# Kernel tuning notes

Measured on AMD Instinct MI355X. Metric: run time of the kernel, lower is better.

The kernel has to match this reference:

```python
import jax, jax.numpy as jnp
import numpy as np

B, S, DMAX, NMEL, DM, K = 8, 100, 12, 80, 128, 9
T = S * DMAX  # 1200 max mel frames
EPS = 1e-5  # BatchNorm eps (eval mode, running_mean=0, running_var=1)


def setup_inputs() -> dict:
    key = jax.random.key(0)
    ks = jax.random.split(key, 16)
    durations = jax.random.randint(ks[0], (B, S), 4, DMAX + 1).astype(jnp.int32)
    mel_len = jnp.sum(durations, axis=1).astype(jnp.int32)
    src_len = jnp.full((B,), S, dtype=jnp.int32)
    mel = jax.random.normal(ks[1], (B, T, NMEL), dtype=jnp.float32)
    # conv stack params (xavier-ish uniform)
    s1 = float(np.sqrt(6.0 / (1 * K + DM * K)))
    w1 = jax.random.uniform(ks[2], (DM, 1, 1, K), minval=-s1, maxval=s1, dtype=jnp.float32)
    g1 = 1.0 + 0.1 * jax.random.normal(ks[3], (DM,), dtype=jnp.float32)
    be1 = 0.1 * jax.random.normal(ks[4], (DM,), dtype=jnp.float32)
    s2 = float(np.sqrt(6.0 / (DM * K + 1 * K)))
    w2 = jax.random.uniform(ks[5], (1, DM, 1, K), minval=-s2, maxval=s2, dtype=jnp.float32)
    g2 = 1.0 + 0.1 * jax.random.normal(ks[6], (1,), dtype=jnp.float32)
    be2 = 0.1 * jax.random.normal(ks[7], (1,), dtype=jnp.float32)
    # BiGRU params (pytorch layout: gates [r|z|n] stacked -> 3*H rows)
    sh = float(1.0 / np.sqrt(DM))
    u = lambda k, shape: jax.random.uniform(k, shape, minval=-sh, maxval=sh, dtype=jnp.float32)
    w_ih_f = u(ks[8], (3 * DM, NMEL)); w_hh_f = u(ks[9], (3 * DM, DM))
    b_ih_f = u(ks[10], (3 * DM,));    b_hh_f = u(ks[11], (3 * DM,))
    w_ih_b = u(ks[12], (3 * DM, NMEL)); w_hh_b = u(ks[13], (3 * DM, DM))
    b_ih_b = u(ks[14], (3 * DM,));    b_hh_b = u(ks[15], (3 * DM,))
    return {"mel": mel, "durations": durations, "mel_len": mel_len, "src_len": src_len,
            "w1": w1, "g1": g1, "be1": be1, "w2": w2, "g2": g2, "be2": be2,
            "w_ih_f": w_ih_f, "w_hh_f": w_hh_f, "b_ih_f": b_ih_f, "b_hh_f": b_hh_f,
            "w_ih_b": w_ih_b, "w_hh_b": w_hh_b, "b_ih_b": b_ih_b, "b_hh_b": b_hh_b}


def _bn_eval(x, g, b):
    # eval-mode BatchNorm2d with running_mean=0, running_var=1; x [B,C,T,M]
    scale = g / jnp.sqrt(1.0 + EPS)
    return x * scale[None, :, None, None] + b[None, :, None, None]


def _gru_scan(xs_seq, reset_seq, w_hh, b_hh):
    # xs_seq [T,B,3H] precomputed input projections; reset_seq [T,B] 1.0 -> reset h to 0
    H = w_hh.shape[1]
    Bn = xs_seq.shape[1]

    def step(h, inp):
        xg, rst = inp
        h = h * (1.0 - rst)[:, None]
        hg = h @ w_hh.T + b_hh
        xr, xz, xn = jnp.split(xg, 3, axis=-1)
        hr, hz, hn = jnp.split(hg, 3, axis=-1)
        r = jax.nn.sigmoid(xr + hr)
        z = jax.nn.sigmoid(xz + hz)
        n = jnp.tanh(xn + r * hn)
        h_new = (1.0 - z) * n + z * h
        return h_new, h_new

    h0 = jnp.zeros((Bn, H), xs_seq.dtype)
    _, hs = jax.lax.scan(step, h0, (xs_seq, reset_seq))
    return hs  # [T,B,H]


def reference(mel, durations, mel_len, src_len, w1, g1, be1, w2, g2, be2,
              w_ih_f, w_hh_f, b_ih_f, b_hh_f, w_ih_b, w_hh_b, b_ih_b, b_hh_b):
    pad = (K - 1) // 2
    # conv stack: kernel (1,K) mixes only the mel-channel axis -> apply to full mel once
    x = mel[:, None, :, :]  # [B,1,T,M]
    x = jax.lax.conv_general_dilated(x, w1, (1, 1), [(0, 0), (pad, pad)])
    x = jax.nn.relu(_bn_eval(x, g1, be1))
    x = jax.lax.conv_general_dilated(x, w2, (1, 1), [(0, 0), (pad, pad)])
    x = jax.nn.relu(_bn_eval(x, g2, be2))
    x = x[:, 0]  # [B,T,M]

    # segment boundaries from durations (all phones valid here, durations > 0)
    cum = jnp.cumsum(durations, axis=1)      # [B,S]
    starts = cum - durations                 # segment start frame per phone
    ends = cum - 1                           # segment end frame per phone
    bidx = jnp.arange(B)[:, None]
    start_mask = jnp.zeros((B, T), x.dtype).at[bidx, starts].set(1.0)
    end_mask = jnp.zeros((B, T), x.dtype).at[bidx, ends].set(1.0)

    # forward direction: reset h at segment starts, read h at segment ends
    xf = jnp.einsum('btm,gm->tbg', x, w_ih_f) + b_ih_f
    Hf = _gru_scan(xf, start_mask.T, w_hh_f, b_hh_f)           # [T,B,H]
    # backward direction: scan reversed time, reset at original segment ends
    xb = jnp.einsum('btm,gm->tbg', x, w_ih_b) + b_ih_b
    Hb = _gru_scan(xb[::-1], end_mask.T[::-1], w_hh_b, b_hh_b)[::-1]  # [T,B,H], orig time

    hf = jnp.take_along_axis(jnp.transpose(Hf, (1, 0, 2)), ends[..., None], axis=1)    # [B,S,H]
    hb = jnp.take_along_axis(jnp.transpose(Hb, (1, 0, 2)), starts[..., None], axis=1)  # [B,S,H]
    out = jnp.concatenate([hf, hb], axis=-1)  # [B,S,2H]
    valid = (jnp.arange(S)[None, :] < src_len[:, None])[..., None]
    return jnp.where(valid, out, 0.0)
```

## Files before the change

kernel.cpp:

```cpp
#include <hip/hip_runtime.h>
#include <math.h>

#define BB   8
#define SS   100
#define TT   1200
#define NM   80
#define DMC  128
#define KK   9
#define G3   384
#define NROW (BB*TT)

typedef __attribute__((ext_vector_type(8))) short short8;
typedef __attribute__((ext_vector_type(4))) float f32x4;
typedef __attribute__((ext_vector_type(2))) float f32x2;

__device__ __forceinline__ float sigmoid_(float v) { return 1.f / (1.f + __expf(-v)); }
__device__ __forceinline__ float tanh_(float v) {
    float a = fabsf(v);
    float e = __expf(-2.f * a);
    float t = (1.f - e) / (1.f + e);
    return copysignf(t, v);
}
__device__ __forceinline__ unsigned short f2bf(float f) {
    unsigned int u = __float_as_uint(f);
    unsigned int r = (u + 0x7fffu + ((u >> 16) & 1u)) >> 16;
    return (unsigned short)r;
}
__device__ __forceinline__ f32x2 pk_fma(f32x2 a, f32x2 b, f32x2 c) {
    f32x2 d;
    asm("v_pk_fma_f32 %0, %1, %2, %3" : "=v"(d) : "v"(a), "v"(b), "v"(c));
    return d;
}
__device__ __forceinline__ f32x2 pk_add(f32x2 a, f32x2 b) {
    f32x2 d;
    asm("v_pk_add_f32 %0, %1, %2" : "=v"(d) : "v"(a), "v"(b));
    return d;
}

__global__ __launch_bounds__(256) void k_convprep(
    const float* __restrict__ mel, const int* __restrict__ mel_len,
    const float* __restrict__ w1, const float* __restrict__ g1, const float* __restrict__ be1,
    const float* __restrict__ w2, const float* __restrict__ g2, const float* __restrict__ be2,
    float* __restrict__ xout,
    const float* __restrict__ whf, const float* __restrict__ whb,
    const float* __restrict__ wif, const float* __restrict__ wib,
    const float* __restrict__ bf, const float* __restrict__ bbv,
    const int* __restrict__ dur,
    unsigned short* __restrict__ wph, unsigned short* __restrict__ wpl,
    unsigned short* __restrict__ wih_h, unsigned short* __restrict__ wih_l,
    float* __restrict__ biasc, int* __restrict__ starts) {
    int bx = blockIdx.x;
    int b  = blockIdx.y;
    int tid = threadIdx.x;

    if (bx >= 600) {
        int pid = (bx - 600) * 8 + b;
        if (pid < 87) {
            int u = pid * 256 + tid;
            if (u < 12288) {
                int idx = u;
                int lane = idx & 63;
                int k32  = (idx >> 6) & 3;
                int tau  = (idx >> 8) % 24;
                int dir  = idx / (24 * 4 * 64);
                const float* w = dir ? whb : whf;
                int gg = tau * 16 + (lane & 15);
                int kbase = k32 * 32 + (lane >> 4) * 8;
#pragma unroll
                for (int j = 0; j < 8; j++) {
                    float v = w[gg * DMC + kbase + j];
                    unsigned short hi = f2bf(v);
                    float hif = __uint_as_float(((unsigned)hi) << 16);
                    unsigned short lo = f2bf(v - hif);
                    wph[idx * 8 + j] = hi;
                    wpl[idx * 8 + j] = lo;
                }
            } else if (u < 21504) {
                int idx = u - 12288;
                int lane = idx & 63;
                int ks   = (idx >> 6) % 3;
                int tau  = idx / (3 * 64);
                int gate = tau * 16 + (lane & 15);
                int kb   = ks * 32 + (lane >> 4) * 8;
                const float* w = (gate < G3) ? (wif + gate * NM) : (wib + (gate - G3) * NM);
#pragma unroll
                for (int j = 0; j < 8; j++) {
                    int k = kb + j;
                    float v = (k < NM) ? w[k] : 0.f;
                    unsigned short hi = f2bf(v);
                    float hif = __uint_as_float(((unsigned)hi) << 16);
                    unsigned short lo = f2bf(v - hif);
                    wih_h[idx * 8 + j] = hi;
                    wih_l[idx * 8 + j] = lo;
                }
            } else {
                int v = u - 21504;
                biasc[v] = (v < G3) ? bf[v] : bbv[v - G3];
            }
        } else {
            int batch = tid >> 5, l = tid & 31;
            int run = 0;
#pragma unroll
            for (int c = 0; c < 4; c++) {
                int s = c * 32 + l;
                int v = (s < SS) ? dur[batch * SS + s] : 0;
                int xv = v;
#pragma unroll
                for (int off = 1; off < 32; off <<= 1) {
                    int t = __shfl_up(xv, off, 32);
                    if (l >= off) xv += t;
                }
                if (s < SS) starts[batch * SS + s] = run + xv - v;
                run += __shfl(xv, 31, 32);
            }
        }
        return;
    }

    int t0 = bx * 2;
    int ml = mel_len[b];
    if (t0 >= ml) return;

    __shared__ __align__(16) f32x2 mp2[96];
    __shared__ __align__(16) f32x2 part2[8][82];

    int mq = tid >> 6, g = tid & 63;
    int ms = 20 * mq;
    const float inv_sqrt = 0.9999950000374997f;

    if (tid < 192) {
        int rr = tid / 96, i = tid - rr * 96;
        float v = 0.f;
        if (i >= 8 && i < 88) v = mel[(b * TT + t0 + rr) * NM + i - 8];
        ((float*)mp2)[i * 2 + rr] = v;
    }
    __syncthreads();

    f32x2 c[20];
#pragma unroll
    for (int m = 0; m < 20; m++) c[m] = (f32x2){0.f, 0.f};

#pragma unroll 1
    for (int dd = 0; dd < 2; dd++) {
        int d = g + 64 * dd;
        float sc = g1[d] * inv_sqrt;
        f32x2 w1p[KK], w2p[KK];
#pragma unroll
        for (int k = 0; k < KK; k++) {
            float a  = w1[d * KK + k] * sc;
            float bq = w2[d * KK + k];
            w1p[k] = (f32x2){a, a};
            w2p[k] = (f32x2){bq, bq};
        }
        float sb = be1[d];
        f32x2 sbp = (f32x2){sb, sb};

        f32x2 mw[12];
        {
            const float4* p4 = (const float4*)(mp2 + ms);
#pragma unroll
            for (int q = 0; q < 6; q++) {
                float4 v = p4[q];
                mw[2 * q]     = (f32x2){v.x, v.y};
                mw[2 * q + 1] = (f32x2){v.z, v.w};
            }
        }
#pragma unroll
        for (int ch = 0; ch < 7; ch++) {
            bool live = true;
            if (ch == 0) live = (mq != 0);
            if (ch == 6) live = (mq != 3);
            if (live) {
                f32x2 yv4[4];
#pragma unroll
                for (int jj = 0; jj < 4; jj++) {
                    f32x2 yv = sbp;
#pragma unroll
                    for (int k = 0; k < KK; k++) yv = pk_fma(w1p[k], mw[jj + k], yv);
                    yv[0] = fmaxf(yv[0], 0.f);
                    yv[1] = fmaxf(yv[1], 0.f);
                    yv4[jj] = yv;
                }
#pragma unroll
                for (int jj = 0; jj < 4; jj++) {
                    int off = ch * 4 + jj;
#pragma unroll
                    for (int k = 0; k < KK; k++) {
                        int mo = off - k;
                        if (mo >= 0 && mo < 20) c[mo] = pk_fma(w2p[k], yv4[jj], c[mo]);
                    }
                }
            }
            if (ch < 6) {
#pragma unroll
                for (int q = 0; q < 8; q++) mw[q] = mw[q + 4];
                const float4* p4 = (const float4*)(mp2 + ms + ch * 4 + 12);
                float4 a0 = p4[0], a1 = p4[1];
                mw[8]  = (f32x2){a0.x, a0.y};
                mw[9]  = (f32x2){a0.z, a0.w};
                mw[10] = (f32x2){a1.x, a1.y};
                mw[11] = (f32x2){a1.z, a1.w};
            }
        }
    }

#pragma unroll
    for (int m = 0; m < 20; m++) {
        f32x2 o;
        o[0] = __shfl_xor(c[m][0], 1);
        o[1] = __shfl_xor(c[m][1], 1);
        c[m] = pk_add(c[m], o);
        o[0] = __shfl_xor(c[m][0], 2);
        o[1] = __shfl_xor(c[m][1], 2);
        c[m] = pk_add(c[m], o);
        o[0] = __shfl_xor(c[m][0], 4);
        o[1] = __shfl_xor(c[m][1], 4);
        c[m] = pk_add(c[m], o);
    }
    if ((g & 7) == 0) {
        int p = g >> 3;
#pragma unroll
        for (int m = 0; m < 20; m++) part2[p][ms + m] = c[m];
    }
    __syncthreads();

    if (tid < 160) {
        int rr = (tid >= 80) ? 1 : 0;
        int m  = tid - 80 * rr;
        int t  = t0 + rr;
        if (t < ml) {
            float s = 0.f;
#pragma unroll
            for (int p = 0; p < 8; p++) s += part2[p][m][rr];
            float v = fmaxf(0.f, fmaf(s, g2[0] * inv_sqrt, be2[0]));
            xout[(b * TT + t) * NM + m] = v;
        }
    }
}

__global__ __launch_bounds__(512, 2) void k_gru(
    const float* __restrict__ x,
    const unsigned short* __restrict__ wph, const unsigned short* __restrict__ wpl,
    const unsigned short* __restrict__ wih_h, const unsigned short* __restrict__ wih_l,
    const float* __restrict__ biasc,
    const int* __restrict__ dur_all, const int* __restrict__ starts,
    const int* __restrict__ src_len,
    const float* __restrict__ bhf, const float* __restrict__ bhb,
    float* __restrict__ out) {
    int sblk = blockIdx.x;
    int b    = blockIdx.y;
    int dir  = blockIdx.z;
    int s0 = sblk * 16;

    __shared__ __align__(16) short8 xbh[12][192];
    __shared__ __align__(16) short8 xbl[12][192];
    __shared__ __align__(16) unsigned short hbh[2][2048];
    __shared__ __align__(16) unsigned short hbl[2][2048];
    __shared__ int sdur[16], sstart[16];

    int tid  = threadIdx.x;
    int wave = tid >> 6, lane = tid & 63;
    int quad = lane >> 4, seg = lane & 15;

    if (tid < 16) {
        int ss = s0 + tid;
        sdur[tid]   = (ss < SS) ? dur_all[b * SS + ss] : 0;
        sstart[tid] = (ss < SS) ? starts[b * SS + ss]  : 0;
    }
    for (int i = tid; i < 2048; i += 512) { hbh[0][i] = 0; hbl[0][i] = 0; }

    short8 Ah[3][4], Al[3][4];
    const short8* wph8 = (const short8*)wph;
    const short8* wpl8 = (const short8*)wpl;
#pragma unroll
    for (int tt = 0; tt < 3; tt++)
#pragma unroll
        for (int k32 = 0; k32 < 4; k32++) {
            int idx = ((dir * 24 + wave + 8 * tt) * 4 + k32) * 64 + lane;
            Ah[tt][k32] = wph8[idx];
            Al[tt][k32] = wpl8[idx];
        }
    short8 Gh[3][3], Gl[3][3];
    const short8* wih_h8 = (const short8*)wih_h;
    const short8* wih_l8 = (const short8*)wih_l;
#pragma unroll
    for (int tt = 0; tt < 3; tt++)
#pragma unroll
        for (int ks = 0; ks < 3; ks++) {
            int idx = ((dir * 24 + wave + 8 * tt) * 3 + ks) * 64 + lane;
            Gh[tt][ks] = wih_h8[idx];
            Gl[tt][ks] = wih_l8[idx];
        }

    int s = s0 + seg;
    int sd = (s < SS) ? dur_all[b * SS + s] : 0;
    int slb = src_len[b];
    const float* bih = biasc + dir * G3;
    const float* bhh = dir ? bhb : bhf;
    int j0 = wave * 16 + quad * 4;
    float4 i_r = *(const float4*)&bih[j0];
    float4 i_z = *(const float4*)&bih[DMC + j0];
    float4 bxn = *(const float4*)&bih[2 * DMC + j0];
    float4 h_r = *(const float4*)&bhh[j0];
    float4 h_z = *(const float4*)&bhh[DMC + j0];
    float4 bhn = *(const float4*)&bhh[2 * DMC + j0];
    float4 br = make_float4(i_r.x + h_r.x, i_r.y + h_r.y, i_r.z + h_r.z, i_r.w + h_r.w);
    float4 bz = make_float4(i_z.x + h_z.x, i_z.y + h_z.y, i_z.z + h_z.z, i_z.w + h_z.w);
    float4 h = make_float4(0.f, 0.f, 0.f, 0.f);

    int idx8 = (j0 >> 5) * 64 + ((j0 >> 3) & 3) * 16 + seg;
    int wbase = idx8 * 8 + (j0 & 7);

    __syncthreads();

#pragma unroll
    for (int q = 0; q < 5; q++) {
        int u = tid + q * 512;
        if (u < 12 * 192) {
            int it  = u / 192;
            int rem = u - it * 192;
            int ks = rem >> 6, ln = rem & 63;
            int sg = ln & 15, qq = ln >> 4;
            int kb = ks * 32 + qq * 8;
            short8 hi8 = {0,0,0,0,0,0,0,0}, lo8 = {0,0,0,0,0,0,0,0};
            int d2 = sdur[sg];
            if (kb < NM && it < d2) {
                int t = dir ? (sstart[sg] + d2 - 1 - it) : (sstart[sg] + it);
                const float* xr = x + (size_t)(b * TT + t) * NM + kb;
#pragma unroll
                for (int j = 0; j < 8; j++) {
                    float v = xr[j];
                    unsigned short hi = f2bf(v);
                    hi8[j] = (short)hi;
                    lo8[j] = (short)f2bf(v - __uint_as_float(((unsigned)hi) << 16));
                }
            }
            xbh[it][rem] = hi8;
            xbl[it][rem] = lo8;
        }
    }
    __syncthreads();

    for (int i = 0; i < 12; i++) {
        int p = i & 1;
        bool act = (i < sd);

        f32x4 axr = (f32x4){0.f,0.f,0.f,0.f};
        f32x4 axz = (f32x4){0.f,0.f,0.f,0.f};
        f32x4 axn = (f32x4){0.f,0.f,0.f,0.f};
        f32x4 ahr = (f32x4){0.f,0.f,0.f,0.f};
        f32x4 ahz = (f32x4){0.f,0.f,0.f,0.f};
        f32x4 ahn = (f32x4){0.f,0.f,0.f,0.f};
#pragma unroll
        for (int ks = 0; ks < 3; ks++) {
            short8 Bxh = xbh[i][ks * 64 + lane];
            short8 Bxl = xbl[i][ks * 64 + lane];
            axr = __builtin_amdgcn_mfma_f32_16x16x32_bf16(Gh[0][ks], Bxh, axr, 0, 0, 0);
            axr = __builtin_amdgcn_mfma_f32_16x16x32_bf16(Gh[0][ks], Bxl, axr, 0, 0, 0);
            axr = __builtin_amdgcn_mfma_f32_16x16x32_bf16(Gl[0][ks], Bxh, axr, 0, 0, 0);
            axz = __builtin_amdgcn_mfma_f32_16x16x32_bf16(Gh[1][ks], Bxh, axz, 0, 0, 0);
            axz = __builtin_amdgcn_mfma_f32_16x16x32_bf16(Gh[1][ks], Bxl, axz, 0, 0, 0);
            axz = __builtin_amdgcn_mfma_f32_16x16x32_bf16(Gl[1][ks], Bxh, axz, 0, 0, 0);
            axn = __builtin_amdgcn_mfma_f32_16x16x32_bf16(Gh[2][ks], Bxh, axn, 0, 0, 0);
            axn = __builtin_amdgcn_mfma_f32_16x16x32_bf16(Gh[2][ks], Bxl, axn, 0, 0, 0);
            axn = __builtin_amdgcn_mfma_f32_16x16x32_bf16(Gl[2][ks], Bxh, axn, 0, 0, 0);
        }
#pragma unroll
        for (int k32 = 0; k32 < 4; k32++) {
            short8 Bh = ((const short8*)hbh[p])[k32 * 64 + lane];
            short8 Bl = ((const short8*)hbl[p])[k32 * 64 + lane];
            ahr = __builtin_amdgcn_mfma_f32_16x16x32_bf16(Ah[0][k32], Bh, ahr, 0, 0, 0);
            ahr = __builtin_amdgcn_mfma_f32_16x16x32_bf16(Ah[0][k32], Bl, ahr, 0, 0, 0);
            ahr = __builtin_amdgcn_mfma_f32_16x16x32_bf16(Al[0][k32], Bh, ahr, 0, 0, 0);
            ahz = __builtin_amdgcn_mfma_f32_16x16x32_bf16(Ah[1][k32], Bh, ahz, 0, 0, 0);
            ahz = __builtin_amdgcn_mfma_f32_16x16x32_bf16(Ah[1][k32], Bl, ahz, 0, 0, 0);
            ahz = __builtin_amdgcn_mfma_f32_16x16x32_bf16(Al[1][k32], Bh, ahz, 0, 0, 0);
            ahn = __builtin_amdgcn_mfma_f32_16x16x32_bf16(Ah[2][k32], Bh, ahn, 0, 0, 0);
            ahn = __builtin_amdgcn_mfma_f32_16x16x32_bf16(Ah[2][k32], Bl, ahn, 0, 0, 0);
            ahn = __builtin_amdgcn_mfma_f32_16x16x32_bf16(Al[2][k32], Bh, ahn, 0, 0, 0);
        }

        if (act) {
            float hv[4]  = {h.x, h.y, h.z, h.w};
            float brv[4] = {br.x, br.y, br.z, br.w};
            float bzv[4] = {bz.x, bz.y, bz.z, bz.w};
            float bxv[4] = {bxn.x, bxn.y, bxn.z, bxn.w};
            float bhv[4] = {bhn.x, bhn.y, bhn.z, bhn.w};
#pragma unroll
            for (int cmp = 0; cmp < 4; cmp++) {
                float r = sigmoid_(axr[cmp] + ahr[cmp] + brv[cmp]);
                float z = sigmoid_(axz[cmp] + ahz[cmp] + bzv[cmp]);
                float n = tanh_(axn[cmp] + bxv[cmp] + r * (ahn[cmp] + bhv[cmp]));
                hv[cmp] = (1.f - z) * n + z * hv[cmp];
            }
            h = make_float4(hv[0], hv[1], hv[2], hv[3]);
            if (i == sd - 1) {
                float4 vout = (s < slb) ? h : make_float4(0.f, 0.f, 0.f, 0.f);
                *(float4*)&out[(b * SS + s) * (2 * DMC) + dir * DMC + j0] = vout;
            }
        }

        {
            float hv[4] = {h.x, h.y, h.z, h.w};
            unsigned short hs_[4], ls_[4];
#pragma unroll
            for (int cmp = 0; cmp < 4; cmp++) {
                unsigned short hi = f2bf(hv[cmp]);
                float hif = __uint_as_float(((unsigned)hi) << 16);
                hs_[cmp] = hi;
                ls_[cmp] = f2bf(hv[cmp] - hif);
            }
            *(ushort4*)&hbh[1 - p][wbase] = make_ushort4(hs_[0], hs_[1], hs_[2], hs_[3]);
            *(ushort4*)&hbl[1 - p][wbase] = make_ushort4(ls_[0], ls_[1], ls_[2], ls_[3]);
        }
        __syncthreads();
    }
}

extern "C" void kernel_launch(void* const* d_in, const int* in_sizes, int n_in,
                              void* d_out, int out_size, void* d_ws, size_t ws_size,
                              hipStream_t stream) {
    const float* mel      = (const float*)d_in[0];
    const int*   durations= (const int*)  d_in[1];
    const int*   mel_len  = (const int*)  d_in[2];
    const int*   src_len  = (const int*)  d_in[3];
    const float* w1       = (const float*)d_in[4];
    const float* g1       = (const float*)d_in[5];
    const float* be1      = (const float*)d_in[6];
    const float* w2       = (const float*)d_in[7];
    const float* g2       = (const float*)d_in[8];
    const float* be2      = (const float*)d_in[9];
    const float* w_ih_f   = (const float*)d_in[10];
    const float* w_hh_f   = (const float*)d_in[11];
    const float* b_ih_f   = (const float*)d_in[12];
    const float* b_hh_f   = (const float*)d_in[13];
    const float* w_ih_b   = (const float*)d_in[14];
    const float* w_hh_b   = (const float*)d_in[15];
    const float* b_ih_b   = (const float*)d_in[16];
    const float* b_hh_b   = (const float*)d_in[17];
    float* out = (float*)d_out;

    float* x    = (float*)d_ws;
    unsigned short* wph   = (unsigned short*)(x + NROW * NM);
    unsigned short* wpl   = wph + 2 * 24 * 4 * 64 * 8;
    unsigned short* wih_h = wpl + 2 * 24 * 4 * 64 * 8;
    unsigned short* wih_l = wih_h + 48 * 3 * 64 * 8;
    float* biasc = (float*)(wih_l + 48 * 3 * 64 * 8);
    int*   starts= (int*)(biasc + 768);

    k_convprep<<<dim3(611, BB), 256, 0, stream>>>(
        mel, mel_len, w1, g1, be1, w2, g2, be2, x,
        w_hh_f, w_hh_b, w_ih_f, w_ih_b, b_ih_f, b_ih_b,
        durations, wph, wpl, wih_h, wih_l, biasc, starts);
    k_gru<<<dim3(7, 8, 2), 512, 0, stream>>>(x, wph, wpl, wih_h, wih_l, biasc,
                                             durations, starts, src_len,
                                             b_hh_f, b_hh_b, out);
}
```

Baseline: 154.3 us.

## Fuse conv and GRU stages into one persistent cooperative kernel

Merges the conv-stack/weight-prep kernel and the BiGRU kernel into a single cooperative launch of 256 persistent 512-thread blocks. Each block loops over frame pairs for the conv, with the conv weights held in registers across iterations, then a subset of blocks runs the GRU after a grid-wide sync. The shared memory of the two phases is overlaid in a union. This removes one kernel launch and the gap between the two kernels, and reuses the per-channel conv weights across rows. In exchange it needs a grid barrier, and the GRU phase only occupies 112 of the 256 blocks.

Result: slower. 277.6 us (+80.0%).

```diff
diff --git a/kernel.cpp b/kernel.cpp
--- a/kernel.cpp
+++ b/kernel.cpp
@@ -1,5 +1,8 @@
 #include <hip/hip_runtime.h>
+#include <hip/hip_cooperative_groups.h>
 #include <math.h>
+
+namespace cg = cooperative_groups;
 
 #define BB   8
 #define SS   100
@@ -37,7 +40,20 @@
     return d;
 }
 
-__global__ __launch_bounds__(256) void k_convprep(
+struct ConvSh {
+    f32x2 mp2[2][96];
+    f32x2 part2[2][8][82];
+};
+struct GruSh {
+    short8 xbh[12][192];
+    short8 xbl[12][192];
+    unsigned short hbh[2][2048];
+    unsigned short hbl[2][2048];
+    int sdur[16], sstart[16];
+};
+union SharedU { ConvSh cv; GruSh gr; };
+
+__global__ __launch_bounds__(512, 2) void k_fused(
     const float* __restrict__ mel, const int* __restrict__ mel_len,
     const float* __restrict__ w1, const float* __restrict__ g1, const float* __restrict__ be1,
     const float* __restrict__ w2, const float* __restrict__ g2, const float* __restrict__ be2,
@@ -48,372 +64,373 @@
     const int* __restrict__ dur,
     unsigned short* __restrict__ wph, unsigned short* __restrict__ wpl,
     unsigned short* __restrict__ wih_h, unsigned short* __restrict__ wih_l,
-    float* __restrict__ biasc, int* __restrict__ starts) {
-    int bx = blockIdx.x;
-    int b  = blockIdx.y;
-    int tid = threadIdx.x;
-
-    if (bx >= 600) {
-        int pid = (bx - 600) * 8 + b;
-        if (pid < 87) {
-            int u = pid * 256 + tid;
-            if (u < 12288) {
-                int idx = u;
-                int lane = idx & 63;
-                int k32  = (idx >> 6) & 3;
-                int tau  = (idx >> 8) % 24;
-                int dir  = idx / (24 * 4 * 64);
-                const float* w = dir ? whb : whf;
-                int gg = tau * 16 + (lane & 15);
-                int kbase = k32 * 32 + (lane >> 4) * 8;
-#pragma unroll
-                for (int j = 0; j < 8; j++) {
-                    float v = w[gg * DMC + kbase + j];
-                    unsigned short hi = f2bf(v);
-                    float hif = __uint_as_float(((unsigned)hi) << 16);
-                    unsigned short lo = f2bf(v - hif);
-                    wph[idx * 8 + j] = hi;
-                    wpl[idx * 8 + j] = lo;
-                }
-            } else if (u < 21504) {
-                int idx = u - 12288;
-                int lane = idx & 63;
-                int ks   = (idx >> 6) % 3;
-                int tau  = idx / (3 * 64);
-                int gate = tau * 16 + (lane & 15);
-                int kb   = ks * 32 + (lane >> 4) * 8;
-                const float* w = (gate < G3) ? (wif + gate * NM) : (wib + (gate - G3) * NM);
-#pragma unroll
-                for (int j = 0; j < 8; j++) {
-                    int k = kb + j;
-                    float v = (k < NM) ? w[k] : 0.f;
-                    unsigned short hi = f2bf(v);
-                    float hif = __uint_as_float(((unsigned)hi) << 16);
-                    unsigned short lo = f2bf(v - hif);
-                    wih_h[idx * 8 + j] = hi;
-                    wih_l[idx * 8 + j] = lo;
-                }
-            } else {
-                int v = u - 21504;
-                biasc[v] = (v < G3) ? bf[v] : bbv[v - G3];
-            }
-        } else {
-            int batch = tid >> 5, l = tid & 31;
-            int run = 0;
-#pragma unroll
-            for (int c = 0; c < 4; c++) {
-                int s = c * 32 + l;
-                int v = (s < SS) ? dur[batch * SS + s] : 0;
-                int xv = v;
-#pragma unroll
-                for (int off = 1; off < 32; off <<= 1) {
-                    int t = __shfl_up(xv, off, 32);
-                    if (l >= off) xv += t;
-                }
-                if (s < SS) starts[batch * SS + s] = run + xv - v;
-                run += __shfl(xv, 31, 32);
-            }
-        }
-        return;
-    }
-
-    int t0 = bx * 2;
-    int ml = mel_len[b];
-    if (t0 >= ml) return;
-
-    __shared__ __align__(16) f32x2 mp2[96];
-    __shared__ __align__(16) f32x2 part2[8][82];
-
-    int mq = tid >> 6, g = tid & 63;
-    int ms = 20 * mq;
-    const float inv_sqrt = 0.9999950000374997f;
-
-    if (tid < 192) {
-        int rr = tid / 96, i = tid - rr * 96;
-        float v = 0.f;
-        if (i >= 8 && i < 88) v = mel[(b * TT + t0 + rr) * NM + i - 8];
-        ((float*)mp2)[i * 2 + rr] = v;
-    }
-    __syncthreads();
-
-    f32x2 c[20];
-#pragma unroll
-    for (int m = 0; m < 20; m++) c[m] = (f32x2){0.f, 0.f};
-
-#pragma unroll 1
-    for (int dd = 0; dd < 2; dd++) {
-        int d = g + 64 * dd;
-        float sc = g1[d] * inv_sqrt;
-        f32x2 w1p[KK], w2p[KK];
-#pragma unroll
-        for (int k = 0; k < KK; k++) {
-            float a  = w1[d * KK + k] * sc;
-            float bq = w2[d * KK + k];
-            w1p[k] = (f32x2){a, a};
-            w2p[k] = (f32x2){bq, bq};
-        }
-        float sb = be1[d];
-        f32x2 sbp = (f32x2){sb, sb};
-
-        f32x2 mw[12];
-        {
-            const float4* p4 = (const float4*)(mp2 + ms);
-#pragma unroll
-            for (int q = 0; q < 6; q++) {
-                float4 v = p4[q];
-                mw[2 * q]     = (f32x2){v.x, v.y};
-                mw[2 * q + 1] = (f32x2){v.z, v.w};
-            }
-        }
-#pragma unroll
-        for (int ch = 0; ch < 7; ch++) {
-            bool live = true;
-            if (ch == 0) live = (mq != 0);
-            if (ch == 6) live = (mq != 3);
-            if (live) {
-                f32x2 yv4[4];
-#pragma unroll
-                for (int jj = 0; jj < 4; jj++) {
-                    f32x2 yv = sbp;
-#pragma unroll
-                    for (int k = 0; k < KK; k++) yv = pk_fma(w1p[k], mw[jj + k], yv);
-                    yv[0] = fmaxf(yv[0], 0.f);
-                    yv[1] = fmaxf(yv[1], 0.f);
-                    yv4[jj] = yv;
-                }
-#pragma unroll
-                for (int jj = 0; jj < 4; jj++) {
-                    int off = ch * 4 + jj;
-#pragma unroll
-                    for (int k = 0; k < KK; k++) {
-                        int mo = off - k;
-                        if (mo >= 0 && mo < 20) c[mo] = pk_fma(w2p[k], yv4[jj], c[mo]);
-                    }
-                }
-            }
-            if (ch < 6) {
-#pragma unroll
-                for (int q = 0; q < 8; q++) mw[q] = mw[q + 4];
-                const float4* p4 = (const float4*)(mp2 + ms + ch * 4 + 12);
-                float4 a0 = p4[0], a1 = p4[1];
-                mw[8]  = (f32x2){a0.x, a0.y};
-                mw[9]  = (f32x2){a0.z, a0.w};
-                mw[10] = (f32x2){a1.x, a1.y};
-                mw[11] = (f32x2){a1.z, a1.w};
-            }
-        }
-    }
-
-#pragma unroll
-    for (int m = 0; m < 20; m++) {
-        f32x2 o;
-        o[0] = __shfl_xor(c[m][0], 1);
-        o[1] = __shfl_xor(c[m][1], 1);
-        c[m] = pk_add(c[m], o);
-        o[0] = __shfl_xor(c[m][0], 2);
-        o[1] = __shfl_xor(c[m][1], 2);
-        c[m] = pk_add(c[m], o);
-        o[0] = __shfl_xor(c[m][0], 4);
-        o[1] = __shfl_xor(c[m][1], 4);
-        c[m] = pk_add(c[m], o);
-    }
-    if ((g & 7) == 0) {
-        int p = g >> 3;
-#pragma unroll
-        for (int m = 0; m < 20; m++) part2[p][ms + m] = c[m];
-    }
-    __syncthreads();
-
-    if (tid < 160) {
-        int rr = (tid >= 80) ? 1 : 0;
-        int m  = tid - 80 * rr;
-        int t  = t0 + rr;
-        if (t < ml) {
-            float s = 0.f;
-#pragma unroll
-            for (int p = 0; p < 8; p++) s += part2[p][m][rr];
-            float v = fmaxf(0.f, fmaf(s, g2[0] * inv_sqrt, be2[0]));
-            xout[(b * TT + t) * NM + m] = v;
-        }
-    }
-}
-
-__global__ __launch_bounds__(512, 2) void k_gru(
-    const float* __restrict__ x,
-    const unsigned short* __restrict__ wph, const unsigned short* __restrict__ wpl,
-    const unsigned short* __restrict__ wih_h, const unsigned short* __restrict__ wih_l,
-    const float* __restrict__ biasc,
-    const int* __restrict__ dur_all, const int* __restrict__ starts,
+    float* __restrict__ biasc, int* __restrict__ starts,
     const int* __restrict__ src_len,
     const float* __restrict__ bhf, const float* __restrict__ bhb,
     float* __restrict__ out) {
-    int sblk = blockIdx.x;
-    int b    = blockIdx.y;
-    int dir  = blockIdx.z;
-    int s0 = sblk * 16;
-
-    __shared__ __align__(16) short8 xbh[12][192];
-    __shared__ __align__(16) short8 xbl[12][192];
-    __shared__ __align__(16) unsigned short hbh[2][2048];
-    __shared__ __align__(16) unsigned short hbl[2][2048];
-    __shared__ int sdur[16], sstart[16];
-
-    int tid  = threadIdx.x;
-    int wave = tid >> 6, lane = tid & 63;
-    int quad = lane >> 4, seg = lane & 15;
-
-    if (tid < 16) {
-        int ss = s0 + tid;
-        sdur[tid]   = (ss < SS) ? dur_all[b * SS + ss] : 0;
-        sstart[tid] = (ss < SS) ? starts[b * SS + ss]  : 0;
+    int bid = blockIdx.x;
+    int tid = threadIdx.x;
+    __shared__ __align__(16) SharedU sh;
+
+    {
+        int hh = tid >> 8, t2 = tid & 255;
+        int mq = t2 >> 6, g = t2 & 63;
+        int ms = 20 * mq;
+        const float inv_sqrt = 0.9999950000374997f;
+
+        f32x2 w1p[2][KK], w2p[2][KK], sbp[2];
+#pragma unroll
+        for (int dd = 0; dd < 2; dd++) {
+            int d = g + 64 * dd;
+            float sc = g1[d] * inv_sqrt;
+#pragma unroll
+            for (int k = 0; k < KK; k++) {
+                float a  = w1[d * KK + k] * sc;
+                float bq = w2[d * KK + k];
+                w1p[dd][k] = (f32x2){a, a};
+                w2p[dd][k] = (f32x2){bq, bq};
+            }
+            float sb = be1[d];
+            sbp[dd] = (f32x2){sb, sb};
+        }
+        float g2s = g2[0] * inv_sqrt;
+        float be2s = be2[0];
+
+        for (int r = 0; r < 10; r++) {
+            int pr = r * 512 + bid * 2 + hh;
+            int b = 0, t0 = 0, ml = 0;
+            bool live = false;
+            if (pr < 4800) {
+                b  = pr & 7;
+                t0 = (pr >> 3) * 2;
+                ml = mel_len[b];
+                live = (t0 < ml);
+            }
+            if (live && t2 < 192) {
+                int rr = t2 / 96, i = t2 - rr * 96;
+                float v = 0.f;
+                if (i >= 8 && i < 88) v = mel[(b * TT + t0 + rr) * NM + i - 8];
+                ((float*)sh.cv.mp2[hh])[i * 2 + rr] = v;
+            }
+            __syncthreads();
+            if (live) {
+                f32x2 c[20];
+#pragma unroll
+                for (int m = 0; m < 20; m++) c[m] = (f32x2){0.f, 0.f};
+
+#pragma unroll
+                for (int dd = 0; dd < 2; dd++) {
+                    f32x2 mw[12];
+                    {
+                        const float4* p4 = (const float4*)(sh.cv.mp2[hh] + ms);
+#pragma unroll
+                        for (int q = 0; q < 6; q++) {
+                            float4 v = p4[q];
+                            mw[2 * q]     = (f32x2){v.x, v.y};
+                            mw[2 * q + 1] = (f32x2){v.z, v.w};
+                        }
+                    }
+#pragma unroll
+                    for (int ch = 0; ch < 7; ch++) {
+                        bool liveg = true;
+                        if (ch == 0) liveg = (mq != 0);
+                        if (ch == 6) liveg = (mq != 3);
+                        if (liveg) {
+                            f32x2 yv4[4];
+#pragma unroll
+                            for (int jj = 0; jj < 4; jj++) {
+                                f32x2 yv = sbp[dd];
+#pragma unroll
+                                for (int k = 0; k < KK; k++) yv = pk_fma(w1p[dd][k], mw[jj + k], yv);
+                                yv[0] = fmaxf(yv[0], 0.f);
+                                yv[1] = fmaxf(yv[1], 0.f);
+                                yv4[jj] = yv;
+                            }
+#pragma unroll
+                            for (int jj = 0; jj < 4; jj++) {
+                                int off = ch * 4 + jj;
+#pragma unroll
+                                for (int k = 0; k < KK; k++) {
+                                    int mo = off - k;
+                                    if (mo >= 0 && mo < 20) c[mo] = pk_fma(w2p[dd][k], yv4[jj], c[mo]);
+                                }
+                            }
+                        }
+                        if (ch < 6) {
+#pragma unroll
+                            for (int q = 0; q < 8; q++) mw[q] = mw[q + 4];
+                            const float4* p4 = (const float4*)(sh.cv.mp2[hh] + ms + ch * 4 + 12);
+                            float4 a0 = p4[0], a1 = p4[1];
+                            mw[8]  = (f32x2){a0.x, a0.y};
+                            mw[9]  = (f32x2){a0.z, a0.w};
+                            mw[10] = (f32x2){a1.x, a1.y};
+                            mw[11] = (f32x2){a1.z, a1.w};
+                        }
+                    }
+                }
+
+#pragma unroll
+                for (int m = 0; m < 20; m++) {
+                    f32x2 o;
+                    o[0] = __shfl_xor(c[m][0], 1);
+                    o[1] = __shfl_xor(c[m][1], 1);
+                    c[m] = pk_add(c[m], o);
+                    o[0] = __shfl_xor(c[m][0], 2);
+                    o[1] = __shfl_xor(c[m][1], 2);
+                    c[m] = pk_add(c[m], o);
+                    o[0] = __shfl_xor(c[m][0], 4);
+                    o[1] = __shfl_xor(c[m][1], 4);
+                    c[m] = pk_add(c[m], o);
+                }
+                if ((g & 7) == 0) {
+                    int p = g >> 3;
+#pragma unroll
+                    for (int m = 0; m < 20; m++) sh.cv.part2[hh][p][ms + m] = c[m];
+                }
+            }
+            __syncthreads();
+            if (live && t2 < 160) {
+                int rr = (t2 >= 80) ? 1 : 0;
+                int m  = t2 - 80 * rr;
+                int t  = t0 + rr;
+                if (t < ml) {
+                    float s = 0.f;
+#pragma unroll
+                    for (int p = 0; p < 8; p++) s += sh.cv.part2[hh][p][m][rr];
+                    float v = fmaxf(0.f, fmaf(s, g2s, be2s));
+                    xout[(b * TT + t) * NM + m] = v;
+                }
+            }
+        }
     }
-    for (int i = tid; i < 2048; i += 512) { hbh[0][i] = 0; hbl[0][i] = 0; }
-
-    short8 Ah[3][4], Al[3][4];
-    const short8* wph8 = (const short8*)wph;
-    const short8* wpl8 = (const short8*)wpl;
-#pragma unroll
-    for (int tt = 0; tt < 3; tt++)
-#pragma unroll
-        for (int k32 = 0; k32 < 4; k32++) {
-            int idx = ((dir * 24 + wave + 8 * tt) * 4 + k32) * 64 + lane;
-            Ah[tt][k32] = wph8[idx];
-            Al[tt][k32] = wpl8[idx];
-        }
-    short8 Gh[3][3], Gl[3][3];
-    const short8* wih_h8 = (const short8*)wih_h;
-    const short8* wih_l8 = (const short8*)wih_l;
-#pragma unroll
-    for (int tt = 0; tt < 3; tt++)
-#pragma unroll
-        for (int ks = 0; ks < 3; ks++) {
-            int idx = ((dir * 24 + wave + 8 * tt) * 3 + ks) * 64 + lane;
-            Gh[tt][ks] = wih_h8[idx];
-            Gl[tt][ks] = wih_l8[idx];
-        }
-
-    int s = s0 + seg;
-    int sd = (s < SS) ? dur_all[b * SS + s] : 0;
-    int slb = src_len[b];
-    const float* bih = biasc + dir * G3;
-    const float* bhh = dir ? bhb : bhf;
-    int j0 = wave * 16 + quad * 4;
-    float4 i_r = *(const float4*)&bih[j0];
-    float4 i_z = *(const float4*)&bih[DMC + j0];
-    float4 bxn = *(const float4*)&bih[2 * DMC + j0];
-    float4 h_r = *(const float4*)&bhh[j0];
-    float4 h_z = *(const float4*)&bhh[DMC + j0];
-    float4 bhn = *(const float4*)&bhh[2 * DMC + j0];
-    float4 br = make_float4(i_r.x + h_r.x, i_r.y + h_r.y, i_r.z + h_r.z, i_r.w + h_r.w);
-    float4 bz = make_float4(i_z.x + h_z.x, i_z.y + h_z.y, i_z.z + h_z.z, i_z.w + h_z.w);
-    float4 h = make_float4(0.f, 0.f, 0.f, 0.f);
-
-    int idx8 = (j0 >> 5) * 64 + ((j0 >> 3) & 3) * 16 + seg;
-    int wbase = idx8 * 8 + (j0 & 7);
-
-    __syncthreads();
-
-#pragma unroll
-    for (int q = 0; q < 5; q++) {
-        int u = tid + q * 512;
-        if (u < 12 * 192) {
-            int it  = u / 192;
-            int rem = u - it * 192;
-            int ks = rem >> 6, ln = rem & 63;
-            int sg = ln & 15, qq = ln >> 4;
-            int kb = ks * 32 + qq * 8;
-            short8 hi8 = {0,0,0,0,0,0,0,0}, lo8 = {0,0,0,0,0,0,0,0};
-            int d2 = sdur[sg];
-            if (kb < NM && it < d2) {
-                int t = dir ? (sstart[sg] + d2 - 1 - it) : (sstart[sg] + it);
-                const float* xr = x + (size_t)(b * TT + t) * NM + kb;
-#pragma unroll
-                for (int j = 0; j < 8; j++) {
-                    float v = xr[j];
-                    unsigned short hi = f2bf(v);
-                    hi8[j] = (short)hi;
-                    lo8[j] = (short)f2bf(v - __uint_as_float(((unsigned)hi) << 16));
-                }
-            }
-            xbh[it][rem] = hi8;
-            xbl[it][rem] = lo8;
+
+    if (bid >= 96 && bid < 140) {
+        int u = (bid - 96) * 512 + tid;
+        if (u < 12288) {
+            int idx = u;
+            int lane = idx & 63;
+            int k32  = (idx >> 6) & 3;
+            int tau  = (idx >> 8) % 24;
+            int dirp = idx / (24 * 4 * 64);
+            const float* w = dirp ? whb : whf;
+            int gg = tau * 16 + (lane & 15);
+            int kbase = k32 * 32 + (lane >> 4) * 8;
+#pragma unroll
+            for (int j = 0; j < 8; j++) {
+                float v = w[gg * DMC + kbase + j];
+                unsigned short hi = f2bf(v);
+                float hif = __uint_as_float(((unsigned)hi) << 16);
+                unsigned short lo = f2bf(v - hif);
+                wph[idx * 8 + j] = hi;
+                wpl[idx * 8 + j] = lo;
+            }
+        } else if (u < 21504) {
+            int idx = u - 12288;
+            int lane = idx & 63;
+            int ks   = (idx >> 6) % 3;
+            int tau  = idx / (3 * 64);
+            int gate = tau * 16 + (lane & 15);
+            int kb   = ks * 32 + (lane >> 4) * 8;
+            const float* w = (gate < G3) ? (wif + gate * NM) : (wib + (gate - G3) * NM);
+#pragma unroll
+            for (int j = 0; j < 8; j++) {
+                int k = kb + j;
+                float v = (k < NM) ? w[k] : 0.f;
+                unsigned short hi = f2bf(v);
+                float hif = __uint_as_float(((unsigned)hi) << 16);
+                unsigned short lo = f2bf(v - hif);
+                wih_h[idx * 8 + j] = hi;
+                wih_l[idx * 8 + j] = lo;
+            }
+        } else if (u < 22272) {
+            int v = u - 21504;
+            biasc[v] = (v < G3) ? bf[v] : bbv[v - G3];
+        }
+    } else if (bid == 140 && tid < 256) {
+        int batch = tid >> 5, l = tid & 31;
+        int run = 0;
+#pragma unroll
+        for (int cch = 0; cch < 4; cch++) {
+            int s = cch * 32 + l;
+            int v = (s < SS) ? dur[batch * SS + s] : 0;
+            int xv = v;
+#pragma unroll
+            for (int off = 1; off < 32; off <<= 1) {
+                int t = __shfl_up(xv, off, 32);
+                if (l >= off) xv += t;
+            }
+            if (s < SS) starts[batch * SS + s] = run + xv - v;
+            run += __shfl(xv, 31, 32);
         }
     }
-    __syncthreads();
-
-    for (int i = 0; i < 12; i++) {
-        int p = i & 1;
-        bool act = (i < sd);
-
-        f32x4 axr = (f32x4){0.f,0.f,0.f,0.f};
-        f32x4 axz = (f32x4){0.f,0.f,0.f,0.f};
-        f32x4 axn = (f32x4){0.f,0.f,0.f,0.f};
-        f32x4 ahr = (f32x4){0.f,0.f,0.f,0.f};
-        f32x4 ahz = (f32x4){0.f,0.f,0.f,0.f};
-        f32x4 ahn = (f32x4){0.f,0.f,0.f,0.f};
-#pragma unroll
-        for (int ks = 0; ks < 3; ks++) {
-            short8 Bxh = xbh[i][ks * 64 + lane];
-            short8 Bxl = xbl[i][ks * 64 + lane];
-            axr = __builtin_amdgcn_mfma_f32_16x16x32_bf16(Gh[0][ks], Bxh, axr, 0, 0, 0);
-            axr = __builtin_amdgcn_mfma_f32_16x16x32_bf16(Gh[0][ks], Bxl, axr, 0, 0, 0);
-            axr = __builtin_amdgcn_mfma_f32_16x16x32_bf16(Gl[0][ks], Bxh, axr, 0, 0, 0);
-            axz = __builtin_amdgcn_mfma_f32_16x16x32_bf16(Gh[1][ks], Bxh, axz, 0, 0, 0);
-            axz = __builtin_amdgcn_mfma_f32_16x16x32_bf16(Gh[1][ks], Bxl, axz, 0, 0, 0);
-            axz = __builtin_amdgcn_mfma_f32_16x16x32_bf16(Gl[1][ks], Bxh, axz, 0, 0, 0);
-            axn = __builtin_amdgcn_mfma_f32_16x16x32_bf16(Gh[2][ks], Bxh, axn, 0, 0, 0);
-            axn = __builtin_amdgcn_mfma_f32_16x16x32_bf16(Gh[2][ks], Bxl, axn, 0, 0, 0);
-            axn = __builtin_amdgcn_mfma_f32_16x16x32_bf16(Gl[2][ks], Bxh, axn, 0, 0, 0);
-        }
-#pragma unroll
-        for (int k32 = 0; k32 < 4; k32++) {
-            short8 Bh = ((const short8*)hbh[p])[k32 * 64 + lane];
-            short8 Bl = ((const short8*)hbl[p])[k32 * 64 + lane];
-            ahr = __builtin_amdgcn_mfma_f32_16x16x32_bf16(Ah[0][k32], Bh, ahr, 0, 0, 0);
-            ahr = __builtin_amdgcn_mfma_f32_16x16x32_bf16(Ah[0][k32], Bl, ahr, 0, 0, 0);
-            ahr = __builtin_amdgcn_mfma_f32_16x16x32_bf16(Al[0][k32], Bh, ahr, 0, 0, 0);
-            ahz = __builtin_amdgcn_mfma_f32_16x16x32_bf16(Ah[1][k32], Bh, ahz, 0, 0, 0);
-            ahz = __builtin_amdgcn_mfma_f32_16x16x32_bf16(Ah[1][k32], Bl, ahz, 0, 0, 0);
-            ahz = __builtin_amdgcn_mfma_f32_16x16x32_bf16(Al[1][k32], Bh, ahz, 0, 0, 0);
-            ahn = __builtin_amdgcn_mfma_f32_16x16x32_bf16(Ah[2][k32], Bh, ahn, 0, 0, 0);
-            ahn = __builtin_amdgcn_mfma_f32_16x16x32_bf16(Ah[2][k32], Bl, ahn, 0, 0, 0);
-            ahn = __builtin_amdgcn_mfma_f32_16x16x32_bf16(Al[2][k32], Bh, ahn, 0, 0, 0);
-        }
-
-        if (act) {
-            float hv[4]  = {h.x, h.y, h.z, h.w};
-            float brv[4] = {br.x, br.y, br.z, br.w};
-            float bzv[4] = {bz.x, bz.y, bz.z, bz.w};
-            float bxv[4] = {bxn.x, bxn.y, bxn.z, bxn.w};
-            float bhv[4] = {bhn.x, bhn.y, bhn.z, bhn.w};
-#pragma unroll
-            for (int cmp = 0; cmp < 4; cmp++) {
-                float r = sigmoid_(axr[cmp] + ahr[cmp] + brv[cmp]);
-                float z = sigmoid_(axz[cmp] + ahz[cmp] + bzv[cmp]);
-                float n = tanh_(axn[cmp] + bxv[cmp] + r * (ahn[cmp] + bhv[cmp]));
-                hv[cmp] = (1.f - z) * n + z * hv[cmp];
-            }
-            h = make_float4(hv[0], hv[1], hv[2], hv[3]);
-            if (i == sd - 1) {
-                float4 vout = (s < slb) ? h : make_float4(0.f, 0.f, 0.f, 0.f);
-                *(float4*)&out[(b * SS + s) * (2 * DMC) + dir * DMC + j0] = vout;
-            }
-        }
-
-        {
-            float hv[4] = {h.x, h.y, h.z, h.w};
-            unsigned short hs_[4], ls_[4];
-#pragma unroll
-            for (int cmp = 0; cmp < 4; cmp++) {
-                unsigned short hi = f2bf(hv[cmp]);
-                float hif = __uint_as_float(((unsigned)hi) << 16);
-                hs_[cmp] = hi;
-                ls_[cmp] = f2bf(hv[cmp] - hif);
-            }
-            *(ushort4*)&hbh[1 - p][wbase] = make_ushort4(hs_[0], hs_[1], hs_[2], hs_[3]);
-            *(ushort4*)&hbl[1 - p][wbase] = make_ushort4(ls_[0], ls_[1], ls_[2], ls_[3]);
-        }
+
+    __threadfence();
+    cg::this_grid().sync();
+
+    if (bid >= 112) return;
+    {
+        int sblk = bid % 7;
+        int rb   = bid / 7;
+        int b    = rb & 7;
+        int dir  = rb >> 3;
+        int s0 = sblk * 16;
+
+        int wave = tid >> 6, lane = tid & 63;
+        int quad = lane >> 4, seg = lane & 15;
+
+        if (tid < 16) {
+            int ss = s0 + tid;
+            sh.gr.sdur[tid]   = (ss < SS) ? dur[b * SS + ss] : 0;
+            sh.gr.sstart[tid] = (ss < SS) ? starts[b * SS + ss] : 0;
+        }
+        for (int i = tid; i < 2048; i += 512) { sh.gr.hbh[0][i] = 0; sh.gr.hbl[0][i] = 0; }
+
+        short8 Ah[3][4], Al[3][4];
+        const short8* wph8 = (const short8*)wph;
+        const short8* wpl8 = (const short8*)wpl;
+#pragma unroll
+        for (int tt = 0; tt < 3; tt++)
+#pragma unroll
+            for (int k32 = 0; k32 < 4; k32++) {
+                int idx = ((dir * 24 + wave + 8 * tt) * 4 + k32) * 64 + lane;
+                Ah[tt][k32] = wph8[idx];
+                Al[tt][k32] = wpl8[idx];
+            }
+        short8 Gh[3][3], Gl[3][3];
+        const short8* wih_h8 = (const short8*)wih_h;
+        const short8* wih_l8 = (const short8*)wih_l;
+#pragma unroll
+        for (int tt = 0; tt < 3; tt++)
+#pragma unroll
+            for (int ks = 0; ks < 3; ks++) {
+                int idx = ((dir * 24 + wave + 8 * tt) * 3 + ks) * 64 + lane;
+                Gh[tt][ks] = wih_h8[idx];
+                Gl[tt][ks] = wih_l8[idx];
+            }
+
+        int s = s0 + seg;
+        int sd = (s < SS) ? dur[b * SS + s] : 0;
+        int slb = src_len[b];
+        const float* bih = biasc + dir * G3;
+        const float* bhh = dir ? bhb : bhf;
+        int j0 = wave * 16 + quad * 4;
+        float4 i_r = *(const float4*)&bih[j0];
+        float4 i_z = *(const float4*)&bih[DMC + j0];
+        float4 bxn = *(const float4*)&bih[2 * DMC + j0];
+        float4 h_r = *(const float4*)&bhh[j0];
+        float4 h_z = *(const float4*)&bhh[DMC + j0];
+        float4 bhn = *(const float4*)&bhh[2 * DMC + j0];
+        float4 br = make_float4(i_r.x + h_r.x, i_r.y + h_r.y, i_r.z + h_r.z, i_r.w + h_r.w);
+        float4 bz = make_float4(i_z.x + h_z.x, i_z.y + h_z.y, i_z.z + h_z.z, i_z.w + h_z.w);
+        float4 h = make_float4(0.f, 0.f, 0.f, 0.f);
+
+        int idx8 = (j0 >> 5) * 64 + ((j0 >> 3) & 3) * 16 + seg;
+        int wbase = idx8 * 8 + (j0 & 7);
+
         __syncthreads();
+
+#pragma unroll
+        for (int q = 0; q < 5; q++) {
+            int u = tid + q * 512;
+            if (u < 12 * 192) {
+                int it  = u / 192;
+                int rem = u - it * 192;
+                int ks = rem >> 6, ln = rem & 63;
+                int sg = ln & 15, qq = ln >> 4;
+                int kb = ks * 32 + qq * 8;
+                short8 hi8 = {0,0,0,0,0,0,0,0}, lo8 = {0,0,0,0,0,0,0,0};
+                int d2 = sh.gr.sdur[sg];
+                if (kb < NM && it < d2) {
+                    int t = dir ? (sh.gr.sstart[sg] + d2 - 1 - it) : (sh.gr.sstart[sg] + it);
+                    const float* xr = xout + (size_t)(b * TT + t) * NM + kb;
+#pragma unroll
+                    for (int j = 0; j < 8; j++) {
+                        float v = xr[j];
+                        unsigned short hi = f2bf(v);
+                        hi8[j] = (short)hi;
+                        lo8[j] = (short)f2bf(v - __uint_as_float(((unsigned)hi) << 16));
+                    }
+                }
+                sh.gr.xbh[it][rem] = hi8;
+                sh.gr.xbl[it][rem] = lo8;
+            }
+        }
+        __syncthreads();
+
+        for (int i = 0; i < 12; i++) {
+            int p = i & 1;
+            bool act = (i < sd);
+
+            f32x4 axr = (f32x4){0.f,0.f,0.f,0.f};
+            f32x4 axz = (f32x4){0.f,0.f,0.f,0.f};
+            f32x4 axn = (f32x4){0.f,0.f,0.f,0.f};
+            f32x4 ahr = (f32x4){0.f,0.f,0.f,0.f};
+            f32x4 ahz = (f32x4){0.f,0.f,0.f,0.f};
+            f32x4 ahn = (f32x4){0.f,0.f,0.f,0.f};
+#pragma unroll
+            for (int ks = 0; ks < 3; ks++) {
+                short8 Bxh = sh.gr.xbh[i][ks * 64 + lane];
+                short8 Bxl = sh.gr.xbl[i][ks * 64 + lane];
+                axr = __builtin_amdgcn_mfma_f32_16x16x32_bf16(Gh[0][ks], Bxh, axr, 0, 0, 0);
+                axr = __builtin_amdgcn_mfma_f32_16x16x32_bf16(Gh[0][ks], Bxl, axr, 0, 0, 0);
+                axr = __builtin_amdgcn_mfma_f32_16x16x32_bf16(Gl[0][ks], Bxh, axr, 0, 0, 0);
+                axz = __builtin_amdgcn_mfma_f32_16x16x32_bf16(Gh[1][ks], Bxh, axz, 0, 0, 0);
+                axz = __builtin_amdgcn_mfma_f32_16x16x32_bf16(Gh[1][ks], Bxl, axz, 0, 0, 0);
+                axz = __builtin_amdgcn_mfma_f32_16x16x32_bf16(Gl[1][ks], Bxh, axz, 0, 0, 0);
+                axn = __builtin_amdgcn_mfma_f32_16x16x32_bf16(Gh[2][ks], Bxh, axn, 0, 0, 0);
+                axn = __builtin_amdgcn_mfma_f32_16x16x32_bf16(Gh[2][ks], Bxl, axn, 0, 0, 0);
+                axn = __builtin_amdgcn_mfma_f32_16x16x32_bf16(Gl[2][ks], Bxh, axn, 0, 0, 0);
+            }
+#pragma unroll
+            for (int k32 = 0; k32 < 4; k32++) {
+                short8 Bh = ((const short8*)sh.gr.hbh[p])[k32 * 64 + lane];
+                short8 Bl = ((const short8*)sh.gr.hbl[p])[k32 * 64 + lane];
+                ahr = __builtin_amdgcn_mfma_f32_16x16x32_bf16(Ah[0][k32], Bh, ahr, 0, 0, 0);
+                ahr = __builtin_amdgcn_mfma_f32_16x16x32_bf16(Ah[0][k32], Bl, ahr, 0, 0, 0);
+                ahr = __builtin_amdgcn_mfma_f32_16x16x32_bf16(Al[0][k32], Bh, ahr, 0, 0, 0);
+                ahz = __builtin_amdgcn_mfma_f32_16x16x32_bf16(Ah[1][k32], Bh, ahz, 0, 0, 0);
+                ahz = __builtin_amdgcn_mfma_f32_16x16x32_bf16(Ah[1][k32], Bl, ahz, 0, 0, 0);
+                ahz = __builtin_amdgcn_mfma_f32_16x16x32_bf16(Al[1][k32], Bh, ahz, 0, 0, 0);
+                ahn = __builtin_amdgcn_mfma_f32_16x16x32_bf16(Ah[2][k32], Bh, ahn, 0, 0, 0);
+                ahn = __builtin_amdgcn_mfma_f32_16x16x32_bf16(Ah[2][k32], Bl, ahn, 0, 0, 0);
+                ahn = __builtin_amdgcn_mfma_f32_16x16x32_bf16(Al[2][k32], Bh, ahn, 0, 0, 0);
+            }
+
+            if (act) {
+                float hv[4]  = {h.x, h.y, h.z, h.w};
+                float brv[4] = {br.x, br.y, br.z, br.w};
+                float bzv[4] = {bz.x, bz.y, bz.z, bz.w};
+                float bxv[4] = {bxn.x, bxn.y, bxn.z, bxn.w};
+                float bhv[4] = {bhn.x, bhn.y, bhn.z, bhn.w};
+#pragma unroll
+                for (int cmp = 0; cmp < 4; cmp++) {
+                    float r = sigmoid_(axr[cmp] + ahr[cmp] + brv[cmp]);
+                    float z = sigmoid_(axz[cmp] + ahz[cmp] + bzv[cmp]);
+                    float n = tanh_(axn[cmp] + bxv[cmp] + r * (ahn[cmp] + bhv[cmp]));
+                    hv[cmp] = (1.f - z) * n + z * hv[cmp];
+                }
+                h = make_float4(hv[0], hv[1], hv[2], hv[3]);
+                if (i == sd - 1) {
+                    float4 vout = (s < slb) ? h : make_float4(0.f, 0.f, 0.f, 0.f);
+                    *(float4*)&out[(b * SS + s) * (2 * DMC) + dir * DMC + j0] = vout;
+                }
+            }
+
+            {
+                float hv[4] = {h.x, h.y, h.z, h.w};
+                unsigned short hs_[4], ls_[4];
+#pragma unroll
+                for (int cmp = 0; cmp < 4; cmp++) {
+                    unsigned short hi = f2bf(hv[cmp]);
+                    float hif = __uint_as_float(((unsigned)hi) << 16);
+                    hs_[cmp] = hi;
+                    ls_[cmp] = f2bf(hv[cmp] - hif);
+                }
+                *(ushort4*)&sh.gr.hbh[1 - p][wbase] = make_ushort4(hs_[0], hs_[1], hs_[2], hs_[3]);
+                *(ushort4*)&sh.gr.hbl[1 - p][wbase] = make_ushort4(ls_[0], ls_[1], ls_[2], ls_[3]);
+            }
+            __syncthreads();
+        }
     }
 }
 
@@ -448,11 +465,21 @@
     float* biasc = (float*)(wih_l + 48 * 3 * 64 * 8);
     int*   starts= (int*)(biasc + 768);
 
-    k_convprep<<<dim3(611, BB), 256, 0, stream>>>(
-        mel, mel_len, w1, g1, be1, w2, g2, be2, x,
-        w_hh_f, w_hh_b, w_ih_f, w_ih_b, b_ih_f, b_ih_b,
-        durations, wph, wpl, wih_h, wih_l, biasc, starts);
-    k_gru<<<dim3(7, 8, 2), 512, 0, stream>>>(x, wph, wpl, wih_h, wih_l, biasc,
-                                             durations, starts, src_len,
-                                             b_hh_f, b_hh_b, out);
-}
+    void* args[] = {
+        (void*)&mel, (void*)&mel_len,
+        (void*)&w1, (void*)&g1, (void*)&be1,
+        (void*)&w2, (void*)&g2, (void*)&be2,
+        (void*)&x,
+        (void*)&w_hh_f, (void*)&w_hh_b,
+        (void*)&w_ih_f, (void*)&w_ih_b,
+        (void*)&b_ih_f, (void*)&b_ih_b,
+        (void*)&durations,
+        (void*)&wph, (void*)&wpl, (void*)&wih_h, (void*)&wih_l,
+        (void*)&biasc, (void*)&starts,
+        (void*)&src_len,
+        (void*)&b_hh_f, (void*)&b_hh_b,
+        (void*)&out
+    };
+    hipLaunchCooperativeKernel((const void*)k_fused, dim3(256), dim3(512),
+                               args, 0, stream);
+}
```
